# Optimization experiments

Hardware: AMD Instinct MI355X
Metric: run time of the kernel (lower is better)

## Reference

```python
import jax, jax.numpy as jnp
import numpy as np

N_NODES = 50000
N_EDGES = 800000
D_IN = 8
D_MODEL = 128
N_CLASSES = 2


def gcn_conv(x, W, b, src, dst, n_nodes):
    # PyG GCNConv: h = x @ W; add self-loops; D^{-1/2} A D^{-1/2} aggregation; + bias
    h = x @ W  # [N, D]
    deg = jax.ops.segment_sum(jnp.ones(src.shape[0], h.dtype), dst, num_segments=n_nodes) + 1.0  # +1 self-loop
    dinv = jax.lax.rsqrt(deg)  # deg >= 1 always
    norm = dinv[src] * dinv[dst]  # [E]
    agg = jax.ops.segment_sum(h[src] * norm[:, None], dst, num_segments=n_nodes)
    agg = agg + h * (dinv * dinv)[:, None]  # self-loop term, norm_ii = dinv_i^2
    return agg + b


def setup_inputs() -> dict:
    key = jax.random.key(0)
    ks = jax.random.split(key, 10)
    x = jax.random.normal(ks[0], (N_NODES, D_IN), jnp.float32)
    edge_index = jax.random.randint(ks[1], (2, N_EDGES), 0, N_NODES, jnp.int64 if jax.config.jax_enable_x64 else jnp.int32)
    def glorot(k, shape):
        lim = np.sqrt(6.0 / (shape[0] + shape[1]))
        return jax.random.uniform(k, shape, jnp.float32, -lim, lim)
    return {
        "x": x,
        "edge_index": edge_index,
        "W1": glorot(ks[2], (D_IN, D_MODEL)),
        "b1": jnp.zeros((D_MODEL,), jnp.float32),
        "W2": glorot(ks[3], (D_MODEL, D_MODEL)),
        "b2": jnp.zeros((D_MODEL,), jnp.float32),
        "Wlin1": glorot(ks[4], (2 * D_MODEL, D_MODEL)),
        "blin1": jnp.zeros((D_MODEL,), jnp.float32),
        "Wfin": glorot(ks[5], (D_MODEL, N_CLASSES)),
        "bfin": jnp.zeros((N_CLASSES,), jnp.float32),
    }


def reference(x, edge_index, W1, b1, W2, b2, Wlin1, blin1, Wfin, bfin):
    src, dst = edge_index[0], edge_index[1]
    n = x.shape[0]
    h = jax.nn.relu(gcn_conv(x, W1, b1, src, dst, n))
    h = jax.nn.relu(gcn_conv(h, W2, b2, src, dst, n))
    xpair = jnp.concatenate((h[src], h[dst]), axis=1)  # [E, 2*D]
    xpair = jax.nn.relu(xpair @ Wlin1 + blin1)
    logits = xpair @ Wfin + bfin  # [E, C]
    return jax.nn.log_softmax(logits, axis=1)
```

## Files before the change

kernel.cpp:

```cpp
#include <hip/hip_runtime.h>
#include <stdint.h>
#include <math.h>

#define D 128

typedef unsigned short u16;
typedef __attribute__((ext_vector_type(8))) short bf16x8;
typedef __attribute__((ext_vector_type(4))) float f32x4;
typedef __attribute__((ext_vector_type(2))) float f32x2;

union BU { uint4 u; bf16x8 s; };

__device__ __forceinline__ unsigned f2bf_pk(float a, float b) {
    union { float f; unsigned u; } x, y; x.f = a; y.f = b;
    unsigned ra = x.u + 0x7FFF + ((x.u >> 16) & 1);
    unsigned rb = y.u + 0x7FFF + ((y.u >> 16) & 1);
    return (ra >> 16) | (rb & 0xFFFF0000u);
}
__device__ __forceinline__ u16 f2bf(float f) {
    union { float f; unsigned u; } x; x.f = f;
    unsigned r = x.u + 0x7FFF + ((x.u >> 16) & 1);
    return (u16)(r >> 16);
}
__device__ __forceinline__ f32x2 bf2f2v(unsigned u) {
    union { unsigned w[2]; f32x2 v; } t;
    t.w[0] = u << 16; t.w[1] = u & 0xFFFF0000u;
    return t.v;
}
__device__ __forceinline__ f32x2 vmax0(f32x2 a) {
    return __builtin_elementwise_max(a, (f32x2)(0.f));
}
__device__ __forceinline__ int padded4(int deg) {
    return (deg + 3) & ~3;
}


__global__ __launch_bounds__(256) void k_degree8(const int* __restrict__ dst, int E,
                                                 int* __restrict__ hist8, int N) {
    int i = blockIdx.x * 256 + threadIdx.x;
    int copy = blockIdx.x & 7;
    int E4 = E >> 2;
    if (i < E4) {
        int4 d = ((const int4*)dst)[i];
        int* h = hist8 + copy * N;
        atomicAdd(&h[d.x], 1);
        atomicAdd(&h[d.y], 1);
        atomicAdd(&h[d.z], 1);
        atomicAdd(&h[d.w], 1);
    }
    if (i == 0) {
        for (int j = E4 * 4; j < E; ++j) atomicAdd(&hist8[dst[j]], 1);
    }
}

__global__ __launch_bounds__(256) void k_xcdoff_bsum(int* __restrict__ hist8, int* __restrict__ degi,
                                                     float* __restrict__ dinv, int* __restrict__ bsum, int N) {
    __shared__ int ws[4];
    int t = threadIdx.x;
    int i = blockIdx.x * 256 + t;
    int pd = 0;
    if (i < N) {
        int run = 0;
#pragma unroll
        for (int j = 0; j < 8; ++j) {
            int c = hist8[j * N + i];
            hist8[j * N + i] = run;
            run += c;
        }
        degi[i] = run;
        dinv[i] = rsqrtf((float)run + 1.0f);
        pd = padded4(run);
    }
    int v = pd;
#pragma unroll
    for (int off = 1; off < 64; off <<= 1) v += __shfl_xor(v, off, 64);
    if ((t & 63) == 0) ws[t >> 6] = v;
    __syncthreads();
    if (t == 0) bsum[blockIdx.x] = ws[0] + ws[1] + ws[2] + ws[3];
}

__global__ __launch_bounds__(1024) void k_boff_wprep(const int* __restrict__ bsum, int* __restrict__ boff,
                                                     int nb, int* __restrict__ prow, int N,
                                                     const float* __restrict__ W2, const float* __restrict__ Wlin,
                                                     unsigned* __restrict__ wswz) {
    int t = threadIdx.x;
    if (blockIdx.x == 0) {
        __shared__ int s[1024];
        s[t] = (t < nb) ? bsum[t] : 0;
        __syncthreads();
        for (int off = 1; off < 1024; off <<= 1) {
            int v = (t >= off) ? s[t - off] : 0;
            __syncthreads();
            s[t] += v;
            __syncthreads();
        }
        if (t < nb) boff[t] = (t == 0) ? 0 : s[t - 1];
        if (t == 0) prow[N] = s[1023];
    } else {
        int tid = (blockIdx.x - 1) * 1024 + t;
        int m = tid >> 13;
        int r = tid & 8191;
        int jp = r & 3;
        int lane = (r >> 2) & 63;
        int ct = (r >> 8) & 7;
        int kc = r >> 11;
        int k0 = kc * 32 + (lane >> 4) * 8 + 2 * jp;
        int n = ct * 16 + (lane & 15);
        const float* srcp = (m == 0) ? W2 : (Wlin + (m - 1) * 16384);
        wswz[tid] = f2bf_pk(srcp[k0 * 128 + n], srcp[(k0 + 1) * 128 + n]);
    }
}

__global__ __launch_bounds__(256) void k_scan_final(const int* __restrict__ degi, const int* __restrict__ boff,
                                                    int* __restrict__ prow, int N) {
    __shared__ int s[256];
    int t = threadIdx.x;
    int i = blockIdx.x * 256 + t;
    int pd = (i < N) ? padded4(degi[i]) : 0;
    s[t] = pd;
    __syncthreads();
    for (int off = 1; off < 256; off <<= 1) {
        int v = (t >= off) ? s[t - off] : 0;
        __syncthreads();
        s[t] += v;
        __syncthreads();
    }
    if (i < N) prow[i] = boff[blockIdx.x] + ((t == 0) ? 0 : s[t - 1]);
}


__global__ __launch_bounds__(256) void k_scatter_fill_xform(
        const int* __restrict__ src, const int* __restrict__ dst, int E,
        const int* __restrict__ prow, int* __restrict__ hist8, const int* __restrict__ degi,
        int2* __restrict__ coleid, int N, int eb4, int nb,
        const float* __restrict__ x, const float* __restrict__ W1,
        const float* __restrict__ dinv, unsigned* __restrict__ g) {
    __shared__ float Ws[8 * D];
    int t = threadIdx.x;
    int b = blockIdx.x;
    if (b < eb4) {
        int i = b * 256 + t;
        int copy = b & 7;
        int E4 = E >> 2;
        if (i < E4) {
            int4 d = ((const int4*)dst)[i];
            int4 s4 = ((const int4*)src)[i];
            int* h = hist8 + copy * N;
            int e = i * 4;
            int off;
            off = atomicAdd(&h[d.x], 1); coleid[prow[d.x] + off] = make_int2(s4.x, e + 0);
            off = atomicAdd(&h[d.y], 1); coleid[prow[d.y] + off] = make_int2(s4.y, e + 1);
            off = atomicAdd(&h[d.z], 1); coleid[prow[d.z] + off] = make_int2(s4.z, e + 2);
            off = atomicAdd(&h[d.w], 1); coleid[prow[d.w] + off] = make_int2(s4.w, e + 3);
        }
        if (i == 0) {
            for (int j = E4 * 4; j < E; ++j) {
                int d = dst[j];
                int off = atomicAdd(&hist8[d], 1);
                coleid[prow[d] + off] = make_int2(src[j], j);
            }
        }
    } else if (b < eb4 + nb) {
        int n = (b - eb4) * 256 + t;
        if (n < N) {
            int lo = prow[n];
            int deg = degi[n];
            int pd = padded4(deg);
            for (int j = deg; j < pd; ++j) coleid[lo + j] = make_int2(N, 0);
        }
        if (b == eb4 && t == 0) {
            int P = prow[N];
            for (int j = 0; j < 16; ++j) coleid[P + j] = make_int2(N, 0);
        }
    } else {
        int xb0 = b - eb4 - nb;
        for (int i = t; i < 8 * D; i += 256) Ws[i] = W1[i];
        __syncthreads();
        int node = xb0 * 4 + (t >> 6);
        int l = t & 63;
        if (node < N) {
            float s0 = 0.f, s1 = 0.f;
#pragma unroll
            for (int k = 0; k < 8; ++k) {
                float xv = x[node * 8 + k];
                s0 += xv * Ws[k * D + 2 * l];
                s1 += xv * Ws[k * D + 2 * l + 1];
            }
            float di = dinv[node];
            g[node * 64 + l] = f2bf_pk(s0 * di, s1 * di);
        }
        if (xb0 == 0 && t < 64) g[(size_t)N * 64 + t] = 0;
    }
}


#define HROW 136

template <bool DUAL>
__global__ __launch_bounds__(256) void k_aggemm(const uint4* __restrict__ g, const int* __restrict__ prow,
                                                const int2* __restrict__ coleid, const float* __restrict__ dinv,
                                                const float* __restrict__ biasH,
                                                const uint4* __restrict__ wB0, const uint4* __restrict__ wB1,
                                                const float* __restrict__ bias1,
                                                u16* __restrict__ out0, u16* __restrict__ out1, int N) {
    __shared__ u16 hs[16 * HROW];
    int t = threadIdx.x;
    int wv = t >> 6;
    int lane = t & 63;
    int sub = lane >> 4;
    int r = lane & 15;
    int base = blockIdx.x * 16;

    for (int nd = 0; nd < 4; ++nd) {
        int i = base + wv * 4 + nd;
        int lrow = wv * 4 + nd;
        if (i < N) {
            f32x2 acc2[4];
#pragma unroll
            for (int j = 0; j < 4; ++j) acc2[j] = (f32x2)(0.f);
            int lo = prow[i], hiP = prow[i + 1];
            int idx = lo + sub;
            int c0 = coleid[idx].x;
            int c1 = (idx + 4 < hiP) ? coleid[idx + 4].x : N;
            int c2 = (idx + 8 < hiP) ? coleid[idx + 8].x : N;
            uint4 v0 = g[c0 * 16 + r];
            uint4 v1 = g[c1 * 16 + r];
            for (int k = lo; k < hiP; k += 4) {
                int c3 = (idx + 12 < hiP) ? coleid[idx + 12].x : N;
                uint4 v2 = g[c2 * 16 + r];
                acc2[0] += bf2f2v(v0.x);
                acc2[1] += bf2f2v(v0.y);
                acc2[2] += bf2f2v(v0.z);
                acc2[3] += bf2f2v(v0.w);
                v0 = v1; v1 = v2; c2 = c3; idx += 4;
            }
#pragma unroll
            for (int j = 0; j < 4; ++j) {
                acc2[j].x += __shfl_xor(acc2[j].x, 16, 64);
                acc2[j].y += __shfl_xor(acc2[j].y, 16, 64);
                acc2[j].x += __shfl_xor(acc2[j].x, 32, 64);
                acc2[j].y += __shfl_xor(acc2[j].y, 32, 64);
            }
            if (sub == 0) {
                uint4 sv = g[i * 16 + r];
                acc2[0] += bf2f2v(sv.x);
                acc2[1] += bf2f2v(sv.y);
                acc2[2] += bf2f2v(sv.z);
                acc2[3] += bf2f2v(sv.w);
                float di = dinv[i];
                float4 b0 = ((const float4*)biasH)[r * 2];
                float4 b1v = ((const float4*)biasH)[r * 2 + 1];
                float r0 = fmaxf(acc2[0].x * di + b0.x, 0.f);
                float r1 = fmaxf(acc2[0].y * di + b0.y, 0.f);
                float r2 = fmaxf(acc2[1].x * di + b0.z, 0.f);
                float r3 = fmaxf(acc2[1].y * di + b0.w, 0.f);
                float r4 = fmaxf(acc2[2].x * di + b1v.x, 0.f);
                float r5 = fmaxf(acc2[2].y * di + b1v.y, 0.f);
                float r6 = fmaxf(acc2[3].x * di + b1v.z, 0.f);
                float r7 = fmaxf(acc2[3].y * di + b1v.w, 0.f);
                uint4 o;
                o.x = f2bf_pk(r0, r1);
                o.y = f2bf_pk(r2, r3);
                o.z = f2bf_pk(r4, r5);
                o.w = f2bf_pk(r6, r7);
                *(uint4*)(hs + lrow * HROW + r * 8) = o;
            }
        } else if (sub == 0) {
            *(uint4*)(hs + lrow * HROW + r * 8) = make_uint4(0, 0, 0, 0);
        }
    }
    __syncthreads();

    int quad = lane >> 4;
    int l15 = lane & 15;
    int ct0 = wv * 2;

    f32x4 accA[2], accB[2];
#pragma unroll
    for (int q = 0; q < 2; ++q) { accA[q] = (f32x4){0.f, 0.f, 0.f, 0.f}; accB[q] = (f32x4){0.f, 0.f, 0.f, 0.f}; }

    const uint4* hrow = (const uint4*)(hs + l15 * HROW);
#pragma unroll
    for (int kc = 0; kc < 4; ++kc) {
        BU a; a.u = hrow[kc * 4 + quad];
#pragma unroll
        for (int q = 0; q < 2; ++q) {
            BU b0; b0.u = wB0[(kc * 8 + ct0 + q) * 64 + lane];
            accA[q] = __builtin_amdgcn_mfma_f32_16x16x32_bf16(a.s, b0.s, accA[q], 0, 0, 0);
            if (DUAL) {
                BU b1; b1.u = wB1[(kc * 8 + ct0 + q) * 64 + lane];
                accB[q] = __builtin_amdgcn_mfma_f32_16x16x32_bf16(a.s, b1.s, accB[q], 0, 0, 0);
            }
        }
    }
#pragma unroll
    for (int reg = 0; reg < 4; ++reg) {
        int node = base + quad * 4 + reg;
        if (node >= N) continue;
        float sc = DUAL ? 1.0f : dinv[node];
#pragma unroll
        for (int q = 0; q < 2; ++q) {
            int colj = (ct0 + q) * 16 + l15;
            out0[(size_t)node * 128 + colj] = f2bf(accA[q][reg] * sc);
            if (DUAL) out1[(size_t)node * 128 + colj] = f2bf(accB[q][reg] + bias1[colj]);
        }
    }
    if (blockIdx.x == 0 && t < 64) ((unsigned*)out0)[(size_t)N * 64 + t] = 0;
}


__global__ __launch_bounds__(256) void k_edge(const uint4* __restrict__ a, const uint4* __restrict__ c,
                                              const int* __restrict__ prow, const int* __restrict__ degi,
                                              const int2* __restrict__ coleid,
                                              const float* __restrict__ Wfin, const float* __restrict__ bfin,
                                              float* __restrict__ out, int N) {
    int wave = (blockIdx.x * blockDim.x + threadIdx.x) >> 6;
    int lane = threadIdx.x & 63;
    if (wave >= N) return;
    int d = wave;
    int g = lane >> 4;
    int r = lane & 15;

    f32x2 wf0v[4], wf1v[4];
    const float4* wvp = (const float4*)Wfin;
#pragma unroll
    for (int q = 0; q < 4; ++q) {
        float4 m = wvp[r * 4 + q];
        wf0v[q] = (f32x2){m.x, m.z};
        wf1v[q] = (f32x2){m.y, m.w};
    }
    float bf0 = bfin[0], bf1 = bfin[1];

    f32x2 cf2[4];
    {
        uint4 cv = c[d * 16 + r];
        cf2[0] = bf2f2v(cv.x);
        cf2[1] = bf2f2v(cv.y);
        cf2[2] = bf2f2v(cv.z);
        cf2[3] = bf2f2v(cv.w);
    }

    int lo = prow[d], hiP = prow[d + 1];
    int deg = degi[d];

    int idx = lo + g;
    int2 q0 = coleid[idx];
    int2 q1 = coleid[idx + 4];
    int c1 = (idx + 4 < hiP) ? q1.x : N;
    int2 q2 = coleid[idx + 8];
    int c2 = (idx + 8 < hiP) ? q2.x : N;
    int e0 = q0.y, e1 = q1.y, e2 = q2.y;
    uint4 v0 = a[q0.x * 16 + r];
    uint4 v1 = a[c1 * 16 + r];

    int rel = g;
    for (int k = lo; k < hiP; k += 4) {
        int2 q3 = coleid[idx + 12];
        int c3 = (idx + 12 < hiP) ? q3.x : N;
        uint4 v2 = a[c2 * 16 + r];
        f32x2 p0v = (f32x2)(0.f), p1v = (f32x2)(0.f);
        f32x2 z;
        z = vmax0(bf2f2v(v0.x) + cf2[0]); p0v += z * wf0v[0]; p1v += z * wf1v[0];
        z = vmax0(bf2f2v(v0.y) + cf2[1]); p0v += z * wf0v[1]; p1v += z * wf1v[1];
        z = vmax0(bf2f2v(v0.z) + cf2[2]); p0v += z * wf0v[2]; p1v += z * wf1v[2];
        z = vmax0(bf2f2v(v0.w) + cf2[3]); p0v += z * wf0v[3]; p1v += z * wf1v[3];
        float p0 = p0v.x + p0v.y;
        float p1 = p1v.x + p1v.y;
        p0 += __shfl_xor(p0, 1, 64);
        p0 += __shfl_xor(p0, 2, 64);
        p0 += __shfl_xor(p0, 4, 64);
        p0 += __shfl_xor(p0, 8, 64);
        p1 += __shfl_xor(p1, 1, 64);
        p1 += __shfl_xor(p1, 2, 64);
        p1 += __shfl_xor(p1, 4, 64);
        p1 += __shfl_xor(p1, 8, 64);
        if (r == 0 && rel < deg) {
            float l0 = p0 + bf0, l1 = p1 + bf1;
            float m = fmaxf(l0, l1);
            float lse = m + __logf(__expf(l0 - m) + __expf(l1 - m));
            *((float2*)(out + 2 * (size_t)e0)) = make_float2(l0 - lse, l1 - lse);
        }
        v0 = v1; v1 = v2;
        e0 = e1; e1 = e2; e2 = q3.y;
        c2 = c3; idx += 4; rel += 4;
    }
}

extern "C" void kernel_launch(void* const* d_in, const int* in_sizes, int n_in,
                              void* d_out, int out_size, void* d_ws, size_t ws_size,
                              hipStream_t stream) {
    const float* x     = (const float*)d_in[0];
    const int*   ei    = (const int*)d_in[1];
    const float* W1    = (const float*)d_in[2];
    const float* b1    = (const float*)d_in[3];
    const float* W2    = (const float*)d_in[4];
    const float* b2    = (const float*)d_in[5];
    const float* Wlin1 = (const float*)d_in[6];
    const float* blin1 = (const float*)d_in[7];
    const float* Wfin  = (const float*)d_in[8];
    const float* bfin  = (const float*)d_in[9];
    float* out = (float*)d_out;

    int N = in_sizes[0] / 8;
    int E = in_sizes[1] / 2;
    const int* src = ei;
    const int* dst = ei + E;
    int nb = (N + 255) / 256;
    int eb4 = (E / 4 + 255) / 256;
    int xb = (N + 3) / 4;

    char* w = (char*)d_ws;
    int* hist8 = (int*)w;     w += (size_t)8 * N * 4;
    int* degi = (int*)w;      w += (size_t)N * 4;
    int* prow = (int*)w;      w += (size_t)(N + 1) * 4;
    float* dinv = (float*)w;  w += (size_t)N * 4;
    int* bsum = (int*)w;      w += (size_t)nb * 4;
    int* boff = (int*)w;      w += (size_t)nb * 4;
    w = (char*)(((uintptr_t)w + 255) & ~(uintptr_t)255);
    int2* coleid = (int2*)w;  w += ((size_t)E + 8 * (size_t)N + 64) * 8;
    unsigned* wswz = (unsigned*)w; w += (size_t)3 * 8192 * 4;
    unsigned* bufG = (unsigned*)w; w += (size_t)(N + 1) * 64 * 4;
    unsigned* bufA = (unsigned*)w; w += (size_t)(N + 1) * 64 * 4;
    unsigned* bufC = (unsigned*)w; w += (size_t)N * 64 * 4;
    unsigned* bufG2 = (unsigned*)w; w += (size_t)(N + 1) * 64 * 4;

    hipMemsetAsync(hist8, 0, (size_t)8 * N * 4, stream);

    k_degree8<<<eb4, 256, 0, stream>>>(dst, E, hist8, N);
    k_xcdoff_bsum<<<nb, 256, 0, stream>>>(hist8, degi, dinv, bsum, N);
    k_boff_wprep<<<25, 1024, 0, stream>>>(bsum, boff, nb, prow, N, W2, Wlin1, wswz);
    k_scan_final<<<nb, 256, 0, stream>>>(degi, boff, prow, N);
    k_scatter_fill_xform<<<eb4 + nb + xb, 256, 0, stream>>>(src, dst, E, prow, hist8, degi,
                                                            coleid, N, eb4, nb, x, W1, dinv, bufG);

    int ablocks = (N + 15) / 16;
    k_aggemm<false><<<ablocks, 256, 0, stream>>>((const uint4*)bufG, prow, coleid, dinv, b1,
                                                 (const uint4*)wswz, nullptr, nullptr,
                                                 (u16*)bufG2, nullptr, N);
    k_aggemm<true><<<ablocks, 256, 0, stream>>>((const uint4*)bufG2, prow, coleid, dinv, b2,
                                                (const uint4*)(wswz + 8192), (const uint4*)(wswz + 16384),
                                                blin1, (u16*)bufA, (u16*)bufC, N);

    k_edge<<<(N + 3) / 4, 256, 0, stream>>>((const uint4*)bufA, (const uint4*)bufC,
                                            prow, degi, coleid, Wfin, bfin, out, N);
}
```

Baseline: 293.1 us.

## Record atomic ranks in degree pass; drop edge ids from CSR; edge-parallel classifier

New measurement: 272.6 us. -7.0%, faster.

```diff
diff --git a/kernel.cpp b/kernel.cpp
--- a/kernel.cpp
+++ b/kernel.cpp
@@ -36,20 +36,22 @@
 
 
 __global__ __launch_bounds__(256) void k_degree8(const int* __restrict__ dst, int E,
-                                                 int* __restrict__ hist8, int N) {
+                                                 int* __restrict__ hist8, int* __restrict__ rank, int N) {
     int i = blockIdx.x * 256 + threadIdx.x;
     int copy = blockIdx.x & 7;
     int E4 = E >> 2;
     if (i < E4) {
         int4 d = ((const int4*)dst)[i];
         int* h = hist8 + copy * N;
-        atomicAdd(&h[d.x], 1);
-        atomicAdd(&h[d.y], 1);
-        atomicAdd(&h[d.z], 1);
-        atomicAdd(&h[d.w], 1);
+        int4 rk;
+        rk.x = atomicAdd(&h[d.x], 1);
+        rk.y = atomicAdd(&h[d.y], 1);
+        rk.z = atomicAdd(&h[d.z], 1);
+        rk.w = atomicAdd(&h[d.w], 1);
+        ((int4*)rank)[i] = rk;
     }
     if (i == 0) {
-        for (int j = E4 * 4; j < E; ++j) atomicAdd(&hist8[dst[j]], 1);
+        for (int j = E4 * 4; j < E; ++j) rank[j] = atomicAdd(&hist8[dst[j]], 1);
     }
 }
 
@@ -112,7 +114,7 @@
 }
 
 __global__ __launch_bounds__(256) void k_scan_final(const int* __restrict__ degi, const int* __restrict__ boff,
-                                                    int* __restrict__ prow, int N) {
+                                                    int* __restrict__ prow, int N, int* __restrict__ hist8) {
     __shared__ int s[256];
     int t = threadIdx.x;
     int i = blockIdx.x * 256 + t;
@@ -125,14 +127,20 @@
         s[t] += v;
         __syncthreads();
     }
-    if (i < N) prow[i] = boff[blockIdx.x] + ((t == 0) ? 0 : s[t - 1]);
+    if (i < N) {
+        int p = boff[blockIdx.x] + ((t == 0) ? 0 : s[t - 1]);
+        prow[i] = p;
+#pragma unroll
+        for (int j = 0; j < 8; ++j) hist8[j * N + i] += p;
+    }
 }
 
 
 __global__ __launch_bounds__(256) void k_scatter_fill_xform(
         const int* __restrict__ src, const int* __restrict__ dst, int E,
-        const int* __restrict__ prow, int* __restrict__ hist8, const int* __restrict__ degi,
-        int2* __restrict__ coleid, int N, int eb4, int nb,
+        const int* __restrict__ prow, const int* __restrict__ hist8, const int* __restrict__ rank,
+        const int* __restrict__ degi,
+        int* __restrict__ colsrc, int N, int eb4, int nb,
         const float* __restrict__ x, const float* __restrict__ W1,
         const float* __restrict__ dinv, unsigned* __restrict__ g) {
     __shared__ float Ws[8 * D];
@@ -145,20 +153,16 @@
         if (i < E4) {
             int4 d = ((const int4*)dst)[i];
             int4 s4 = ((const int4*)src)[i];
-            int* h = hist8 + copy * N;
-            int e = i * 4;
-            int off;
-            off = atomicAdd(&h[d.x], 1); coleid[prow[d.x] + off] = make_int2(s4.x, e + 0);
-            off = atomicAdd(&h[d.y], 1); coleid[prow[d.y] + off] = make_int2(s4.y, e + 1);
-            off = atomicAdd(&h[d.z], 1); coleid[prow[d.z] + off] = make_int2(s4.z, e + 2);
-            off = atomicAdd(&h[d.w], 1); coleid[prow[d.w] + off] = make_int2(s4.w, e + 3);
+            int4 rk = ((const int4*)rank)[i];
+            const int* h = hist8 + copy * N;
+            colsrc[h[d.x] + rk.x] = s4.x;
+            colsrc[h[d.y] + rk.y] = s4.y;
+            colsrc[h[d.z] + rk.z] = s4.z;
+            colsrc[h[d.w] + rk.w] = s4.w;
         }
         if (i == 0) {
-            for (int j = E4 * 4; j < E; ++j) {
-                int d = dst[j];
-                int off = atomicAdd(&hist8[d], 1);
-                coleid[prow[d] + off] = make_int2(src[j], j);
-            }
+            for (int j = E4 * 4; j < E; ++j)
+                colsrc[hist8[dst[j]] + rank[j]] = src[j];
         }
     } else if (b < eb4 + nb) {
         int n = (b - eb4) * 256 + t;
@@ -166,11 +170,11 @@
             int lo = prow[n];
             int deg = degi[n];
             int pd = padded4(deg);
-            for (int j = deg; j < pd; ++j) coleid[lo + j] = make_int2(N, 0);
+            for (int j = deg; j < pd; ++j) colsrc[lo + j] = N;
         }
         if (b == eb4 && t == 0) {
             int P = prow[N];
-            for (int j = 0; j < 16; ++j) coleid[P + j] = make_int2(N, 0);
+            for (int j = 0; j < 16; ++j) colsrc[P + j] = N;
         }
     } else {
         int xb0 = b - eb4 - nb;
@@ -198,7 +202,7 @@
 
 template <bool DUAL>
 __global__ __launch_bounds__(256) void k_aggemm(const uint4* __restrict__ g, const int* __restrict__ prow,
-                                                const int2* __restrict__ coleid, const float* __restrict__ dinv,
+                                                const int* __restrict__ colsrc, const float* __restrict__ dinv,
                                                 const float* __restrict__ biasH,
                                                 const uint4* __restrict__ wB0, const uint4* __restrict__ wB1,
                                                 const float* __restrict__ bias1,
@@ -220,13 +224,13 @@
             for (int j = 0; j < 4; ++j) acc2[j] = (f32x2)(0.f);
             int lo = prow[i], hiP = prow[i + 1];
             int idx = lo + sub;
-            int c0 = coleid[idx].x;
-            int c1 = (idx + 4 < hiP) ? coleid[idx + 4].x : N;
-            int c2 = (idx + 8 < hiP) ? coleid[idx + 8].x : N;
+            int c0 = colsrc[idx];
+            int c1 = (idx + 4 < hiP) ? colsrc[idx + 4] : N;
+            int c2 = (idx + 8 < hiP) ? colsrc[idx + 8] : N;
             uint4 v0 = g[c0 * 16 + r];
             uint4 v1 = g[c1 * 16 + r];
             for (int k = lo; k < hiP; k += 4) {
-                int c3 = (idx + 12 < hiP) ? coleid[idx + 12].x : N;
+                int c3 = (idx + 12 < hiP) ? colsrc[idx + 12] : N;
                 uint4 v2 = g[c2 * 16 + r];
                 acc2[0] += bf2f2v(v0.x);
                 acc2[1] += bf2f2v(v0.y);
@@ -310,16 +314,25 @@
 
 
 __global__ __launch_bounds__(256) void k_edge(const uint4* __restrict__ a, const uint4* __restrict__ c,
-                                              const int* __restrict__ prow, const int* __restrict__ degi,
-                                              const int2* __restrict__ coleid,
+                                              const int* __restrict__ src, const int* __restrict__ dst,
                                               const float* __restrict__ Wfin, const float* __restrict__ bfin,
-                                              float* __restrict__ out, int N) {
-    int wave = (blockIdx.x * blockDim.x + threadIdx.x) >> 6;
-    int lane = threadIdx.x & 63;
-    if (wave >= N) return;
-    int d = wave;
-    int g = lane >> 4;
-    int r = lane & 15;
+                                              float* __restrict__ out, int E) {
+    int t = threadIdx.x;
+    int g = t >> 4;
+    int r = t & 15;
+    int base = blockIdx.x * 32;
+    int e0 = base + g;
+    int e1 = base + 16 + g;
+    bool ok0 = e0 < E, ok1 = e1 < E;
+    int ec0 = ok0 ? e0 : 0;
+    int ec1 = ok1 ? e1 : 0;
+
+    int s0 = src[ec0], d0 = dst[ec0];
+    int s1 = src[ec1], d1 = dst[ec1];
+    uint4 av0 = a[(size_t)s0 * 16 + r];
+    uint4 cv0 = c[(size_t)d0 * 16 + r];
+    uint4 av1 = a[(size_t)s1 * 16 + r];
+    uint4 cv1 = c[(size_t)d1 * 16 + r];
 
     f32x2 wf0v[4], wf1v[4];
     const float4* wvp = (const float4*)Wfin;
@@ -331,58 +344,40 @@
     }
     float bf0 = bfin[0], bf1 = bfin[1];
 
-    f32x2 cf2[4];
-    {
-        uint4 cv = c[d * 16 + r];
-        cf2[0] = bf2f2v(cv.x);
-        cf2[1] = bf2f2v(cv.y);
-        cf2[2] = bf2f2v(cv.z);
-        cf2[3] = bf2f2v(cv.w);
-    }
-
-    int lo = prow[d], hiP = prow[d + 1];
-    int deg = degi[d];
-
-    int idx = lo + g;
-    int2 q0 = coleid[idx];
-    int2 q1 = coleid[idx + 4];
-    int c1 = (idx + 4 < hiP) ? q1.x : N;
-    int2 q2 = coleid[idx + 8];
-    int c2 = (idx + 8 < hiP) ? q2.x : N;
-    int e0 = q0.y, e1 = q1.y, e2 = q2.y;
-    uint4 v0 = a[q0.x * 16 + r];
-    uint4 v1 = a[c1 * 16 + r];
-
-    int rel = g;
-    for (int k = lo; k < hiP; k += 4) {
-        int2 q3 = coleid[idx + 12];
-        int c3 = (idx + 12 < hiP) ? q3.x : N;
-        uint4 v2 = a[c2 * 16 + r];
-        f32x2 p0v = (f32x2)(0.f), p1v = (f32x2)(0.f);
-        f32x2 z;
-        z = vmax0(bf2f2v(v0.x) + cf2[0]); p0v += z * wf0v[0]; p1v += z * wf1v[0];
-        z = vmax0(bf2f2v(v0.y) + cf2[1]); p0v += z * wf0v[1]; p1v += z * wf1v[1];
-        z = vmax0(bf2f2v(v0.z) + cf2[2]); p0v += z * wf0v[2]; p1v += z * wf1v[2];
-        z = vmax0(bf2f2v(v0.w) + cf2[3]); p0v += z * wf0v[3]; p1v += z * wf1v[3];
-        float p0 = p0v.x + p0v.y;
-        float p1 = p1v.x + p1v.y;
-        p0 += __shfl_xor(p0, 1, 64);
-        p0 += __shfl_xor(p0, 2, 64);
-        p0 += __shfl_xor(p0, 4, 64);
-        p0 += __shfl_xor(p0, 8, 64);
-        p1 += __shfl_xor(p1, 1, 64);
-        p1 += __shfl_xor(p1, 2, 64);
-        p1 += __shfl_xor(p1, 4, 64);
-        p1 += __shfl_xor(p1, 8, 64);
-        if (r == 0 && rel < deg) {
-            float l0 = p0 + bf0, l1 = p1 + bf1;
+    f32x2 p0a = (f32x2)(0.f), p1a = (f32x2)(0.f);
+    f32x2 p0b = (f32x2)(0.f), p1b = (f32x2)(0.f);
+    f32x2 z;
+    z = vmax0(bf2f2v(av0.x) + bf2f2v(cv0.x)); p0a += z * wf0v[0]; p1a += z * wf1v[0];
+    z = vmax0(bf2f2v(av0.y) + bf2f2v(cv0.y)); p0a += z * wf0v[1]; p1a += z * wf1v[1];
+    z = vmax0(bf2f2v(av0.z) + bf2f2v(cv0.z)); p0a += z * wf0v[2]; p1a += z * wf1v[2];
+    z = vmax0(bf2f2v(av0.w) + bf2f2v(cv0.w)); p0a += z * wf0v[3]; p1a += z * wf1v[3];
+    z = vmax0(bf2f2v(av1.x) + bf2f2v(cv1.x)); p0b += z * wf0v[0]; p1b += z * wf1v[0];
+    z = vmax0(bf2f2v(av1.y) + bf2f2v(cv1.y)); p0b += z * wf0v[1]; p1b += z * wf1v[1];
+    z = vmax0(bf2f2v(av1.z) + bf2f2v(cv1.z)); p0b += z * wf0v[2]; p1b += z * wf1v[2];
+    z = vmax0(bf2f2v(av1.w) + bf2f2v(cv1.w)); p0b += z * wf0v[3]; p1b += z * wf1v[3];
+
+    float q0 = p0a.x + p0a.y, q1 = p1a.x + p1a.y;
+    float q2 = p0b.x + p0b.y, q3 = p1b.x + p1b.y;
+#pragma unroll
+    for (int off = 1; off < 16; off <<= 1) {
+        q0 += __shfl_xor(q0, off, 64);
+        q1 += __shfl_xor(q1, off, 64);
+        q2 += __shfl_xor(q2, off, 64);
+        q3 += __shfl_xor(q3, off, 64);
+    }
+    if (r == 0) {
+        if (ok0) {
+            float l0 = q0 + bf0, l1 = q1 + bf1;
             float m = fmaxf(l0, l1);
             float lse = m + __logf(__expf(l0 - m) + __expf(l1 - m));
             *((float2*)(out + 2 * (size_t)e0)) = make_float2(l0 - lse, l1 - lse);
         }
-        v0 = v1; v1 = v2;
-        e0 = e1; e1 = e2; e2 = q3.y;
-        c2 = c3; idx += 4; rel += 4;
+        if (ok1) {
+            float l0 = q2 + bf0, l1 = q3 + bf1;
+            float m = fmaxf(l0, l1);
+            float lse = m + __logf(__expf(l0 - m) + __expf(l1 - m));
+            *((float2*)(out + 2 * (size_t)e1)) = make_float2(l0 - lse, l1 - lse);
+        }
     }
 }
 
@@ -411,13 +406,14 @@
 
     char* w = (char*)d_ws;
     int* hist8 = (int*)w;     w += (size_t)8 * N * 4;
+    int* rank = (int*)w;      w += (size_t)E * 4;
     int* degi = (int*)w;      w += (size_t)N * 4;
     int* prow = (int*)w;      w += (size_t)(N + 1) * 4;
     float* dinv = (float*)w;  w += (size_t)N * 4;
     int* bsum = (int*)w;      w += (size_t)nb * 4;
     int* boff = (int*)w;      w += (size_t)nb * 4;
     w = (char*)(((uintptr_t)w + 255) & ~(uintptr_t)255);
-    int2* coleid = (int2*)w;  w += ((size_t)E + 8 * (size_t)N + 64) * 8;
+    int* colsrc = (int*)w;    w += ((size_t)E + 8 * (size_t)N + 64) * 4;
     unsigned* wswz = (unsigned*)w; w += (size_t)3 * 8192 * 4;
     unsigned* bufG = (unsigned*)w; w += (size_t)(N + 1) * 64 * 4;
     unsigned* bufA = (unsigned*)w; w += (size_t)(N + 1) * 64 * 4;
@@ -426,21 +422,21 @@
 
     hipMemsetAsync(hist8, 0, (size_t)8 * N * 4, stream);
 
-    k_degree8<<<eb4, 256, 0, stream>>>(dst, E, hist8, N);
+    k_degree8<<<eb4, 256, 0, stream>>>(dst, E, hist8, rank, N);
     k_xcdoff_bsum<<<nb, 256, 0, stream>>>(hist8, degi, dinv, bsum, N);
     k_boff_wprep<<<25, 1024, 0, stream>>>(bsum, boff, nb, prow, N, W2, Wlin1, wswz);
-    k_scan_final<<<nb, 256, 0, stream>>>(degi, boff, prow, N);
-    k_scatter_fill_xform<<<eb4 + nb + xb, 256, 0, stream>>>(src, dst, E, prow, hist8, degi,
-                                                            coleid, N, eb4, nb, x, W1, dinv, bufG);
+    k_scan_final<<<nb, 256, 0, stream>>>(degi, boff, prow, N, hist8);
+    k_scatter_fill_xform<<<eb4 + nb + xb, 256, 0, stream>>>(src, dst, E, prow, hist8, rank, degi,
+                                                            colsrc, N, eb4, nb, x, W1, dinv, bufG);
 
     int ablocks = (N + 15) / 16;
-    k_aggemm<false><<<ablocks, 256, 0, stream>>>((const uint4*)bufG, prow, coleid, dinv, b1,
+    k_aggemm<false><<<ablocks, 256, 0, stream>>>((const uint4*)bufG, prow, colsrc, dinv, b1,
                                                  (const uint4*)wswz, nullptr, nullptr,
                                                  (u16*)bufG2, nullptr, N);
-    k_aggemm<true><<<ablocks, 256, 0, stream>>>((const uint4*)bufG2, prow, coleid, dinv, b2,
+    k_aggemm<true><<<ablocks, 256, 0, stream>>>((const uint4*)bufG2, prow, colsrc, dinv, b2,
                                                 (const uint4*)(wswz + 8192), (const uint4*)(wswz + 16384),
                                                 blin1, (u16*)bufA, (u16*)bufC, N);
 
-    k_edge<<<(N + 3) / 4, 256, 0, stream>>>((const uint4*)bufA, (const uint4*)bufC,
-                                            prow, degi, coleid, Wfin, bfin, out, N);
-}
+    k_edge<<<(E + 31) / 32, 256, 0, stream>>>((const uint4*)bufA, (const uint4*)bufC,
+                                              src, dst, Wfin, bfin, out, E);
+}
```
